# Performance work log

Measured on AMD Instinct MI355X. Metric: run time of the kernel, lower is better.

The kernel has to match this reference:

```python
import jax, jax.numpy as jnp
import numpy as np

B, S, E, H = 2, 2048, 1024, 16
HD = E // H


def setup_inputs() -> dict:
    key = jax.random.key(0)
    ks = jax.random.split(key, 5)
    scale = 1.0 / np.sqrt(E)
    return {
        "query": jax.random.normal(ks[0], (B, S, E), jnp.float32),
        "key": jax.random.normal(ks[1], (B, S, E), jnp.float32),
        "value": jax.random.normal(ks[2], (B, S, E), jnp.float32),
        "qkv_w": jax.random.normal(ks[3], (3 * E, E), jnp.float32) * scale,
        "qkv_b": jnp.zeros((3 * E,), jnp.float32),
        "out_w": jax.random.normal(ks[4], (E, E), jnp.float32) * scale,
        "out_b": jnp.zeros((E,), jnp.float32),
    }


def reference(query, key, value, qkv_w, qkv_b, out_w, out_b):
    # Fused QKV projection from query (module ignores key/value contents)
    qkv = query @ qkv_w.T + qkv_b                      # [B,S,3E]
    qkv = qkv.reshape(B, S, 3, H, HD)
    q = qkv[:, :, 0].transpose(0, 2, 1, 3)             # [B,H,S,HD]
    k = qkv[:, :, 1].transpose(0, 2, 1, 3)
    v = qkv[:, :, 2].transpose(0, 2, 1, 3)
    scaling = 1.0 / np.sqrt(HD)
    scores = jnp.einsum("bhqd,bhkd->bhqk", q, k) * scaling  # [B,H,S,S]
    probs = jax.nn.softmax(scores, axis=-1)
    ctx = jnp.einsum("bhqk,bhkd->bhqd", probs, v)      # [B,H,S,HD]
    ctx = ctx.transpose(0, 2, 1, 3).reshape(B, S, E)
    return ctx @ out_w.T + out_b
```

## Files before the change

kernel.cpp:

```cpp
#include <hip/hip_runtime.h>
#include <hip/hip_bf16.h>
#include <math.h>

#define BB 2
#define SS 2048
#define EE 1024
#define HH 16
#define HD 64

typedef __bf16 bf16;
typedef __bf16 bf16x8 __attribute__((ext_vector_type(8)));
typedef float floatx4 __attribute__((ext_vector_type(4)));

#define MFMA(a, b, c) __builtin_amdgcn_mfma_f32_16x16x32_bf16(a, b, c, 0, 0, 0)

__device__ inline void async16(const bf16* g, bf16* l) {
    __builtin_amdgcn_global_load_lds(
        (const __attribute__((address_space(1))) void*)g,
        (__attribute__((address_space(3))) void*)l, 16, 0, 0);
}

__global__ __launch_bounds__(256) void cvt3(
    const float* __restrict__ a, const float* __restrict__ b,
    const float* __restrict__ c,
    bf16* __restrict__ oa, bf16* __restrict__ ob, bf16* __restrict__ oc) {
    const long NA = (long)4096 * 1024, NB = (long)3072 * 1024, NC = (long)1024 * 1024;
    const long total = (NA + NB + NC) >> 2;
    long i = (long)blockIdx.x * blockDim.x + threadIdx.x;
    const long stride = (long)gridDim.x * blockDim.x;
    for (; i < total; i += stride) {
        const long e = i << 2;
        const float* src;
        bf16* dst;
        if (e < NA)           { src = a + e;            dst = oa + e; }
        else if (e < NA + NB) { src = b + (e - NA);     dst = ob + (e - NA); }
        else                  { src = c + (e - NA - NB); dst = oc + (e - NA - NB); }
        float4 v = *(const float4*)src;
        union { bf16 h[4]; uint2 u; } t;
        t.h[0] = (bf16)v.x; t.h[1] = (bf16)v.y; t.h[2] = (bf16)v.z; t.h[3] = (bf16)v.w;
        *(uint2*)dst = t.u;
    }
}

__global__ __launch_bounds__(256) void qkv_gemm(
    const bf16* __restrict__ A, const bf16* __restrict__ W,
    const float* __restrict__ bias,
    bf16* __restrict__ Qw, bf16* __restrict__ Kw, bf16* __restrict__ Vtw) {
    __shared__ __align__(16) bf16 As[128 * 64];
    __shared__ __align__(16) bf16 Bs[128 * 64];
    const int tid  = threadIdx.x;
    const int wave = tid >> 6, lane = tid & 63;
    const int quad = lane >> 4, l16 = lane & 15;
    const int wr = wave >> 1, wc = wave & 1;
    const int m0 = blockIdx.y * 128, n0 = blockIdx.x * 128;
    const int lr = lane >> 3;
    const int lc = (lane & 7) * 8;

    const bf16* Ag = A + (long)(m0 + wave * 32 + lr) * 1024 + lc;
    const bf16* Bg = W + (long)(n0 + wave * 32 + lr) * 1024 + lc;
    bf16* Al = As + (wave * 32) * 64 + lane * 8;
    bf16* Bl = Bs + (wave * 32) * 64 + lane * 8;

    floatx4 acc[4][4] = {};

    for (int k0 = 0; k0 < 1024; k0 += 64) {
        __syncthreads();
#pragma unroll
        for (int j = 0; j < 4; ++j) {
            async16(Ag + (long)j * 8 * 1024 + k0, Al + j * 8 * 64);
            async16(Bg + (long)j * 8 * 1024 + k0, Bl + j * 8 * 64);
        }
        __syncthreads();
#pragma unroll
        for (int c = 0; c < 2; ++c) {
            bf16x8 af[4], bfr[4];
#pragma unroll
            for (int mi = 0; mi < 4; ++mi)
                af[mi] = *(const bf16x8*)&As[(wr * 64 + mi * 16 + l16) * 64 + c * 32 + quad * 8];
#pragma unroll
            for (int ni = 0; ni < 4; ++ni)
                bfr[ni] = *(const bf16x8*)&Bs[(wc * 64 + ni * 16 + l16) * 64 + c * 32 + quad * 8];
#pragma unroll
            for (int mi = 0; mi < 4; ++mi)
#pragma unroll
                for (int ni = 0; ni < 4; ++ni)
                    acc[mi][ni] = MFMA(af[mi], bfr[ni], acc[mi][ni]);
        }
    }

#pragma unroll
    for (int mi = 0; mi < 4; ++mi)
#pragma unroll
        for (int ni = 0; ni < 4; ++ni) {
            const int n = n0 + wc * 64 + ni * 16 + l16;
            const float bn = bias[n];
            const int sel = n >> 10;
            const int e = n & 1023, h = e >> 6, d = e & 63;
            if (sel == 2) {
                const int m_base = m0 + wr * 64 + mi * 16 + quad * 4;
                const int b = m_base >> 11, s0 = m_base & 2047;
                union { bf16 h4[4]; uint2 u; } t;
#pragma unroll
                for (int r = 0; r < 4; ++r)
                    t.h4[r] = (bf16)(acc[mi][ni][r] + bn);
                *(uint2*)&Vtw[((long)(b * HH + h) * HD + d) * SS + s0] = t.u;
            } else {
#pragma unroll
                for (int r = 0; r < 4; ++r) {
                    const int m = m0 + wr * 64 + mi * 16 + quad * 4 + r;
                    const int b = m >> 11, s = m & 2047;
                    const float v = acc[mi][ni][r] + bn;
                    if (sel == 0)
                        Qw[((long)(b * HH + h) * SS + s) * HD + d] = (bf16)(v * 0.125f);
                    else
                        Kw[((long)(b * HH + h) * SS + s) * HD + d] = (bf16)v;
                }
            }
        }
}

__global__ __launch_bounds__(256) void attn(
    const bf16* __restrict__ Qw, const bf16* __restrict__ Kw,
    const bf16* __restrict__ Vtw, bf16* __restrict__ ctxw) {
    __shared__ __align__(16) bf16 Kt[64][72];
    __shared__ __align__(16) bf16 Vt[64][72];
    __shared__ __align__(16) bf16 Pl[4][32][72];

    const int tid  = threadIdx.x;
    const int wave = tid >> 6, lane = tid & 63;
    const int quad = lane >> 4, l16 = lane & 15;
    const int qb = blockIdx.x, bh = blockIdx.y;
    const bf16* Qh = Qw  + (long)bh * SS * HD;
    const bf16* Kh = Kw  + (long)bh * SS * HD;
    const bf16* Vh = Vtw + (long)bh * HD * SS;

    const int qbase = qb * 128 + wave * 32;
    bf16x8 qf[2][2];
#pragma unroll
    for (int g = 0; g < 2; ++g)
#pragma unroll
        for (int c = 0; c < 2; ++c)
            qf[g][c] = *(const bf16x8*)&Qh[(long)(qbase + g * 16 + l16) * HD + c * 32 + quad * 8];

    floatx4 ctx[2][4] = {};
    float lrun[2][4] = {{0.f,0.f,0.f,0.f},{0.f,0.f,0.f,0.f}};

    const int srow = tid >> 2;
    const int sc0  = (tid & 3) * 16;

    uint4 kr0, kr1, vr0, vr1;
    {
        const uint4* ks = (const uint4*)&Kh[(long)srow * HD + sc0];
        kr0 = ks[0]; kr1 = ks[1];
        const uint4* vs = (const uint4*)&Vh[(long)srow * SS + sc0];
        vr0 = vs[0]; vr1 = vs[1];
    }

    for (int kt = 0; kt < 32; ++kt) {
        __syncthreads();
        *(uint4*)&Kt[srow][sc0]     = kr0;
        *(uint4*)&Kt[srow][sc0 + 8] = kr1;
        *(uint4*)&Vt[srow][sc0]     = vr0;
        *(uint4*)&Vt[srow][sc0 + 8] = vr1;
        __syncthreads();

        if (kt < 31) {
            const uint4* ks = (const uint4*)&Kh[(long)((kt + 1) * 64 + srow) * HD + sc0];
            kr0 = ks[0]; kr1 = ks[1];
            const uint4* vs = (const uint4*)&Vh[(long)srow * SS + (kt + 1) * 64 + sc0];
            vr0 = vs[0]; vr1 = vs[1];
        }

        floatx4 sf[2][4];
#pragma unroll
        for (int j = 0; j < 4; ++j) {
            bf16x8 kf0 = *(const bf16x8*)&Kt[j * 16 + l16][quad * 8];
            bf16x8 kf1 = *(const bf16x8*)&Kt[j * 16 + l16][32 + quad * 8];
#pragma unroll
            for (int g = 0; g < 2; ++g) {
                floatx4 t = {0.f, 0.f, 0.f, 0.f};
                t = MFMA(qf[g][0], kf0, t);
                sf[g][j] = MFMA(qf[g][1], kf1, t);
            }
        }

#pragma unroll
        for (int g = 0; g < 2; ++g)
#pragma unroll
            for (int j = 0; j < 4; ++j)
#pragma unroll
                for (int r = 0; r < 4; ++r) {
                    const float p = __expf(sf[g][j][r]);
                    sf[g][j][r] = p;
                    lrun[g][r] += p;
                }

#pragma unroll
        for (int g = 0; g < 2; ++g)
#pragma unroll
            for (int j = 0; j < 4; ++j)
#pragma unroll
                for (int r = 0; r < 4; ++r)
                    Pl[wave][g * 16 + quad * 4 + r][j * 16 + l16] = (bf16)sf[g][j][r];

#pragma unroll
        for (int kc = 0; kc < 2; ++kc) {
            bf16x8 vf[4];
#pragma unroll
            for (int dt = 0; dt < 4; ++dt)
                vf[dt] = *(const bf16x8*)&Vt[dt * 16 + l16][kc * 32 + quad * 8];
#pragma unroll
            for (int g = 0; g < 2; ++g) {
                bf16x8 pf = *(const bf16x8*)&Pl[wave][g * 16 + l16][kc * 32 + quad * 8];
#pragma unroll
                for (int dt = 0; dt < 4; ++dt)
                    ctx[g][dt] = MFMA(pf, vf[dt], ctx[g][dt]);
            }
        }
    }

    const int b = bh >> 4, h = bh & 15;
#pragma unroll
    for (int g = 0; g < 2; ++g)
#pragma unroll
        for (int r = 0; r < 4; ++r) {
            float rs = lrun[g][r];
#pragma unroll
            for (int off = 1; off < 16; off <<= 1) rs += __shfl_xor(rs, off, 64);
            const float inv = 1.0f / rs;
            const int qg = qbase + g * 16 + quad * 4 + r;
#pragma unroll
            for (int dt = 0; dt < 4; ++dt) {
                const int d = dt * 16 + l16;
                ctxw[((long)b * SS + qg) * EE + h * HD + d] = (bf16)(ctx[g][dt][r] * inv);
            }
        }
}

__global__ __launch_bounds__(256) void out_gemm(
    const bf16* __restrict__ A, const bf16* __restrict__ W,
    const float* __restrict__ bias, float* __restrict__ out) {
    __shared__ __align__(16) bf16 As[64 * 64];
    __shared__ __align__(16) bf16 Bs[128 * 64];
    const int tid  = threadIdx.x;
    const int wave = tid >> 6, lane = tid & 63;
    const int quad = lane >> 4, l16 = lane & 15;
    const int wr = wave & 1, wc = wave >> 1;
    const int m0 = blockIdx.y * 64, n0 = blockIdx.x * 128;
    const int lr = lane >> 3;
    const int lc = (lane & 7) * 8;

    const bf16* Ag = A + (long)(m0 + wave * 16 + lr) * 1024 + lc;
    const bf16* Bg = W + (long)(n0 + wave * 32 + lr) * 1024 + lc;
    bf16* Al = As + (wave * 16) * 64 + lane * 8;
    bf16* Bl = Bs + (wave * 32) * 64 + lane * 8;

    floatx4 acc[2][4] = {};

    for (int k0 = 0; k0 < 1024; k0 += 64) {
        __syncthreads();
#pragma unroll
        for (int j = 0; j < 2; ++j)
            async16(Ag + (long)j * 8 * 1024 + k0, Al + j * 8 * 64);
#pragma unroll
        for (int j = 0; j < 4; ++j)
            async16(Bg + (long)j * 8 * 1024 + k0, Bl + j * 8 * 64);
        __syncthreads();
#pragma unroll
        for (int c = 0; c < 2; ++c) {
            bf16x8 af[2], bfr[4];
#pragma unroll
            for (int mi = 0; mi < 2; ++mi)
                af[mi] = *(const bf16x8*)&As[(wr * 32 + mi * 16 + l16) * 64 + c * 32 + quad * 8];
#pragma unroll
            for (int ni = 0; ni < 4; ++ni)
                bfr[ni] = *(const bf16x8*)&Bs[(wc * 64 + ni * 16 + l16) * 64 + c * 32 + quad * 8];
#pragma unroll
            for (int mi = 0; mi < 2; ++mi)
#pragma unroll
                for (int ni = 0; ni < 4; ++ni)
                    acc[mi][ni] = MFMA(af[mi], bfr[ni], acc[mi][ni]);
        }
    }

#pragma unroll
    for (int mi = 0; mi < 2; ++mi)
#pragma unroll
        for (int ni = 0; ni < 4; ++ni) {
            const int n = n0 + wc * 64 + ni * 16 + l16;
            const float bn = bias[n];
#pragma unroll
            for (int r = 0; r < 4; ++r) {
                const int m = m0 + wr * 32 + mi * 16 + quad * 4 + r;
                out[(long)m * 1024 + n] = acc[mi][ni][r] + bn;
            }
        }
}

extern "C" void kernel_launch(void* const* d_in, const int* in_sizes, int n_in,
                              void* d_out, int out_size, void* d_ws, size_t ws_size,
                              hipStream_t stream) {
    const float* query = (const float*)d_in[0];
    const float* qkv_w = (const float*)d_in[3];
    const float* qkv_b = (const float*)d_in[4];
    const float* out_w = (const float*)d_in[5];
    const float* out_b = (const float*)d_in[6];

    const long NTOK = (long)BB * SS;
    bf16* qb   = (bf16*)d_ws;
    bf16* wqb  = qb  + NTOK * EE;
    bf16* owb  = wqb + (long)3 * EE * EE;
    bf16* Qw   = owb + (long)EE * EE;
    bf16* Kw   = Qw  + NTOK * EE;
    bf16* Vtw  = Kw  + NTOK * EE;
    bf16* ctxw = qb;
    float* out = (float*)d_out;

    cvt3<<<2048, 256, 0, stream>>>(query, qkv_w, out_w, qb, wqb, owb);
    qkv_gemm<<<dim3(24, 32), 256, 0, stream>>>(qb, wqb, qkv_b, Qw, Kw, Vtw);
    attn<<<dim3(16, 32), 256, 0, stream>>>(Qw, Kw, Vtw, ctxw);
    out_gemm<<<dim3(8, 64), 256, 0, stream>>>(ctxw, owb, out_b, out);
}
```

Measured before the change: 234.7 us.

## Load K/V MFMA fragments directly from global memory, drop LDS staging and barriers

```diff
diff --git a/kernel.cpp b/kernel.cpp
--- a/kernel.cpp
+++ b/kernel.cpp
@@ -119,11 +119,9 @@
         }
 }
 
-__global__ __launch_bounds__(256) void attn(
+__global__ __launch_bounds__(256, 2) void attn(
     const bf16* __restrict__ Qw, const bf16* __restrict__ Kw,
     const bf16* __restrict__ Vtw, bf16* __restrict__ ctxw) {
-    __shared__ __align__(16) bf16 Kt[64][72];
-    __shared__ __align__(16) bf16 Vt[64][72];
     __shared__ __align__(16) bf16 Pl[4][32][72];
 
     const int tid  = threadIdx.x;
@@ -145,44 +143,34 @@
     floatx4 ctx[2][4] = {};
     float lrun[2][4] = {{0.f,0.f,0.f,0.f},{0.f,0.f,0.f,0.f}};
 
-    const int srow = tid >> 2;
-    const int sc0  = (tid & 3) * 16;
-
-    uint4 kr0, kr1, vr0, vr1;
-    {
-        const uint4* ks = (const uint4*)&Kh[(long)srow * HD + sc0];
-        kr0 = ks[0]; kr1 = ks[1];
-        const uint4* vs = (const uint4*)&Vh[(long)srow * SS + sc0];
-        vr0 = vs[0]; vr1 = vs[1];
-    }
-
+    const bf16* kbase = Kh + (long)l16 * HD + quad * 8;
+    const bf16* vbase = Vh + (long)l16 * SS + quad * 8;
+
+#pragma unroll 1
     for (int kt = 0; kt < 32; ++kt) {
-        __syncthreads();
-        *(uint4*)&Kt[srow][sc0]     = kr0;
-        *(uint4*)&Kt[srow][sc0 + 8] = kr1;
-        *(uint4*)&Vt[srow][sc0]     = vr0;
-        *(uint4*)&Vt[srow][sc0 + 8] = vr1;
-        __syncthreads();
-
-        if (kt < 31) {
-            const uint4* ks = (const uint4*)&Kh[(long)((kt + 1) * 64 + srow) * HD + sc0];
-            kr0 = ks[0]; kr1 = ks[1];
-            const uint4* vs = (const uint4*)&Vh[(long)srow * SS + (kt + 1) * 64 + sc0];
-            vr0 = vs[0]; vr1 = vs[1];
-        }
+        const int key0 = kt * 64;
+
+        bf16x8 kf[4][2], vf[2][4];
+#pragma unroll
+        for (int j = 0; j < 4; ++j) {
+            kf[j][0] = *(const bf16x8*)(kbase + (long)(key0 + j * 16) * HD);
+            kf[j][1] = *(const bf16x8*)(kbase + (long)(key0 + j * 16) * HD + 32);
+        }
+#pragma unroll
+        for (int kc = 0; kc < 2; ++kc)
+#pragma unroll
+            for (int dt = 0; dt < 4; ++dt)
+                vf[kc][dt] = *(const bf16x8*)(vbase + (long)(dt * 16) * SS + key0 + kc * 32);
 
         floatx4 sf[2][4];
 #pragma unroll
-        for (int j = 0; j < 4; ++j) {
-            bf16x8 kf0 = *(const bf16x8*)&Kt[j * 16 + l16][quad * 8];
-            bf16x8 kf1 = *(const bf16x8*)&Kt[j * 16 + l16][32 + quad * 8];
+        for (int j = 0; j < 4; ++j)
 #pragma unroll
             for (int g = 0; g < 2; ++g) {
                 floatx4 t = {0.f, 0.f, 0.f, 0.f};
-                t = MFMA(qf[g][0], kf0, t);
-                sf[g][j] = MFMA(qf[g][1], kf1, t);
-            }
-        }
+                t = MFMA(qf[g][0], kf[j][0], t);
+                sf[g][j] = MFMA(qf[g][1], kf[j][1], t);
+            }
 
 #pragma unroll
         for (int g = 0; g < 2; ++g)
@@ -204,19 +192,14 @@
                     Pl[wave][g * 16 + quad * 4 + r][j * 16 + l16] = (bf16)sf[g][j][r];
 
 #pragma unroll
-        for (int kc = 0; kc < 2; ++kc) {
-            bf16x8 vf[4];
-#pragma unroll
-            for (int dt = 0; dt < 4; ++dt)
-                vf[dt] = *(const bf16x8*)&Vt[dt * 16 + l16][kc * 32 + quad * 8];
+        for (int kc = 0; kc < 2; ++kc)
 #pragma unroll
             for (int g = 0; g < 2; ++g) {
                 bf16x8 pf = *(const bf16x8*)&Pl[wave][g * 16 + l16][kc * 32 + quad * 8];
 #pragma unroll
                 for (int dt = 0; dt < 4; ++dt)
-                    ctx[g][dt] = MFMA(pf, vf[dt], ctx[g][dt]);
-            }
-        }
+                    ctx[g][dt] = MFMA(pf, vf[kc][dt], ctx[g][dt]);
+            }
     }
 
     const int b = bh >> 4, h = bh & 15;
```

Result: slower. 290.5 us (+23.8%).
